# Optimization experiments

Hardware: AMD Instinct MI355X
Metric: run time of the kernel (lower is better)

The kernel has to match this reference:

```python
import jax, jax.numpy as jnp
import numpy as np

B, T, C = 4, 1024, 768
H, HD = 12, 64
E, K, DFF = 16, 2, 3072
EPS = 1e-5


def layernorm(x, w, b):
    mu = jnp.mean(x, axis=-1, keepdims=True)
    xc = x - mu
    var = jnp.mean(xc * xc, axis=-1, keepdims=True)
    return xc * jax.lax.rsqrt(var + EPS) * w + b


def setup_inputs() -> dict:
    key = jax.random.key(0)
    ks = jax.random.split(key, 12)
    s = lambda fan_in: 1.0 / np.sqrt(fan_in)
    return {
        "x": jax.random.normal(ks[0], (B, T, C), jnp.float32),
        "ln1_w": jnp.ones((C,), jnp.float32),
        "ln1_b": jnp.zeros((C,), jnp.float32),
        "W_attn": jax.random.normal(ks[1], (C, 3 * C), jnp.float32) * s(C),
        "b_attn": jnp.zeros((3 * C,), jnp.float32),
        "W_proj": jax.random.normal(ks[2], (C, C), jnp.float32) * s(C),
        "b_proj": jnp.zeros((C,), jnp.float32),
        "ln2_w": jnp.ones((C,), jnp.float32),
        "ln2_b": jnp.zeros((C,), jnp.float32),
        "W_router": jax.random.normal(ks[3], (C, E), jnp.float32) * s(C),
        "W1": jax.random.normal(ks[4], (E, C, DFF), jnp.float32) * s(C),
        "b1": jnp.zeros((E, DFF), jnp.float32),
        "W2": jax.random.normal(ks[5], (E, DFF, C), jnp.float32) * s(DFF),
        "b2": jnp.zeros((E, C), jnp.float32),
    }


def reference(x, ln1_w, ln1_b, W_attn, b_attn, W_proj, b_proj,
              ln2_w, ln2_b, W_router, W1, b1, W2, b2):
    # --- attention sublayer ---
    xn = layernorm(x, ln1_w, ln1_b)
    qkv = xn @ W_attn + b_attn                                  # [B,T,3C]
    q, k, v = jnp.split(qkv, 3, axis=-1)
    q = q.reshape(B, T, H, HD).transpose(0, 2, 1, 3)            # [B,H,T,HD]
    k = k.reshape(B, T, H, HD).transpose(0, 2, 1, 3)
    v = v.reshape(B, T, H, HD).transpose(0, 2, 1, 3)
    att = jnp.einsum('bhqd,bhkd->bhqk', q, k) / np.sqrt(HD)
    causal = jnp.tril(jnp.ones((T, T), bool))
    att = jnp.where(causal, att, -jnp.inf)
    att = jax.nn.softmax(att, axis=-1)
    y = jnp.einsum('bhqk,bhkd->bhqd', att, v)
    y = y.transpose(0, 2, 1, 3).reshape(B, T, C)
    x = x + y @ W_proj + b_proj

    # --- MoE sublayer: dense all-experts with top-k gating mask ---
    xn2 = layernorm(x, ln2_w, ln2_b)
    probs = jax.nn.softmax(xn2 @ W_router, axis=-1)             # [B,T,E]
    top_p, top_idx = jax.lax.top_k(probs, K)                    # [B,T,K]
    gating = jnp.sum(jax.nn.one_hot(top_idx, E, dtype=probs.dtype)
                     * top_p[..., None], axis=-2)               # [B,T,E]
    g = jnp.moveaxis(gating, -1, 0)                             # [E,B,T]

    def body(acc, params):
        W1e, b1e, W2e, b2e, ge = params
        h = jax.nn.gelu(xn2 @ W1e + b1e, approximate=False)     # [B,T,DFF]
        out = h @ W2e + b2e                                     # [B,T,C]
        return acc + ge[..., None] * out, None

    y_moe, _ = jax.lax.scan(body, jnp.zeros_like(x), (W1, b1, W2, b2, g))
    # note: MoELayer returns x + y, and Block adds residual again
    return x + (xn2_residual := 0) + xn2 * 0 + (x * 0) + x * 0 + y_moe + x * 0 if False else x + (x * 0) + y_moe + x * 0 * 0 if False else x + x * 0 + y_moe + (x - x) if False else x + (x + y_moe) - x + (x + y_moe) - (x + y_moe) if False else x + x + y_moe - x if False else (x + (x + y_moe)) - x + (x - x) if False else x + y_moe + x - x if False else _block_out(x, xn2, y_moe)


def _block_out(x, xn2, y_moe):
    # MoELayer.forward returns x_in + y where x_in is ln2 *input* (x here);
    # Block then does x = x + ffn(ln2(x)) -> x + (x + y_moe)? No: MoE input is
    # xn2 = ln2(x), so ffn(ln2(x)) = xn2 + y_moe, and Block adds residual x.
    return x + xn2 + y_moe
```

## Files before the change

### kernel.cpp

```cpp
#include <hip/hip_runtime.h>
#include <math.h>

#define CC    768
#define C3    2304
#define KD    2304
#define LDA2  1536
#define TT    1024
#define BB    4
#define HH    12
#define HD    64
#define EE    16
#define DFFN  3072
#define NTOK  4096
#define NSLOT 8192
#define LDP   136

typedef unsigned short u16;
typedef unsigned int   u32;
typedef __attribute__((ext_vector_type(8))) short short8;
typedef __attribute__((ext_vector_type(4))) float floatx4;

__device__ __forceinline__ u16 f2bf(float f){
  u32 x = __builtin_bit_cast(u32, f);
  x += 0x7fffu + ((x >> 16) & 1u);
  return (u16)(x >> 16);
}
__device__ __forceinline__ u16 f2h(float f){
  _Float16 h = (_Float16)f;
  return __builtin_bit_cast(u16, h);
}
__device__ __forceinline__ float h2f(u16 u){
  return (float)__builtin_bit_cast(_Float16, u);
}
__device__ __forceinline__ float gelu_exact(float v){
  return 0.5f * v * (1.f + erff(v * 0.70710678118654752440f));
}
__device__ __forceinline__ void split2h(float v, u16& h0, u16& h1){
  float vs = v * 64.f;
  h0 = f2h(vs);
  h1 = f2h(vs - h2f(h0));
}
__device__ __forceinline__ void gload_lds16(const void* g, void* l){
  __builtin_amdgcn_global_load_lds(
      (const __attribute__((address_space(1))) void*)g,
      (__attribute__((address_space(3))) void*)l, 16, 0, 0);
}

#define PIPE_WAIT_STEADY  asm volatile("s_waitcnt vmcnt(4) lgkmcnt(0)" ::: "memory")
#define PIPE_WAIT_LAST    asm volatile("s_waitcnt vmcnt(0) lgkmcnt(0)" ::: "memory")
#define PIPE_BARRIER      asm volatile("s_barrier" ::: "memory")

template<int MODE>
__global__ __launch_bounds__(256) void transpose_split(const float* __restrict__ src,
    u16* __restrict__ d0, int R, int Cn)
{
  __shared__ float tile[32][33];
  int z = blockIdx.z;
  const float* s = src + (size_t)z * R * Cn;
  int c0 = blockIdx.x * 32, r0 = blockIdx.y * 32;
  int tx = threadIdx.x & 31, ty = threadIdx.x >> 5;
  #pragma unroll
  for (int j = 0; j < 4; ++j)
    tile[ty + j*8][tx] = s[(size_t)(r0 + ty + j*8) * Cn + c0 + tx];
  __syncthreads();
  #pragma unroll
  for (int j = 0; j < 4; ++j){
    float v = tile[tx][ty + j*8];
    if (MODE == 1){
      u16 h0, h1; split2h(v, h0, h1);
      size_t base = (size_t)(c0 + ty + j*8) * LDA2 + (r0 + tx);
      d0[base] = h0; d0[base + 768] = h1;
    } else {
      d0[(size_t)z * R * Cn + (size_t)(c0 + ty + j*8) * R + r0 + tx] = f2bf(v);
    }
  }
}

template<int MODE>
__global__ __launch_bounds__(256) void ln_kernel(const float* __restrict__ x,
    const float* __restrict__ gw, const float* __restrict__ gb,
    float* __restrict__ of, u16* __restrict__ o0)
{
  int tok = blockIdx.x, tid = threadIdx.x;
  const float* xr = x + (size_t)tok * CC;
  float v0 = xr[tid], v1 = xr[tid + 256], v2 = xr[tid + 512];
  __shared__ float r1[4], r2[4];
  __shared__ float mus, rss;
  float s = v0 + v1 + v2;
  #pragma unroll
  for (int off = 32; off >= 1; off >>= 1) s += __shfl_down(s, off);
  if ((tid & 63) == 0) r1[tid >> 6] = s;
  __syncthreads();
  if (tid == 0) mus = (r1[0] + r1[1] + r1[2] + r1[3]) * (1.f / 768.f);
  __syncthreads();
  float mu = mus;
  float d0 = v0 - mu, d1 = v1 - mu, d2 = v2 - mu;
  float t = d0*d0 + d1*d1 + d2*d2;
  #pragma unroll
  for (int off = 32; off >= 1; off >>= 1) t += __shfl_down(t, off);
  if ((tid & 63) == 0) r2[tid >> 6] = t;
  __syncthreads();
  if (tid == 0) rss = rsqrtf((r2[0] + r2[1] + r2[2] + r2[3]) * (1.f / 768.f) + 1e-5f);
  __syncthreads();
  float rstd = rss;
  float dv[3] = {d0, d1, d2};
  #pragma unroll
  for (int i = 0; i < 3; ++i){
    int c = tid + i * 256;
    float vv = dv[i] * rstd * gw[c] + gb[c];
    if (MODE == 1){
      u16 h0, h1; split2h(vv, h0, h1);
      o0[(size_t)tok * LDA2 + c] = h0;
      o0[(size_t)tok * LDA2 + 768 + c] = h1;
    } else {
      size_t idx = (size_t)tok * CC + c;
      of[idx] = vv;
      o0[idx] = f2bf(vv);
    }
  }
}

__global__ __launch_bounds__(256) void gemm_dense(
    const u16* __restrict__ A, const u16* __restrict__ Bt,
    float* __restrict__ C, const float* __restrict__ bias,
    const float* __restrict__ resid, int N)
{
  __shared__ u16 As[3][128 * 32];
  __shared__ u16 Bs[3][128 * 32];
  int tid = threadIdx.x;
  int lane = tid & 63, wave = tid >> 6;
  int wm = wave & 1, wn = wave >> 1;
  int m0 = blockIdx.y * 128, n0 = blockIdx.x * 128;
  int ra = tid >> 2, ka = (tid & 3) * 8;
  const u16* pa0 = A  + (size_t)(m0 + ra)      * LDA2 + ka;
  const u16* pa1 = A  + (size_t)(m0 + ra + 64) * LDA2 + ka;
  const u16* pb0 = Bt + (size_t)(n0 + ra)      * LDA2 + ka;
  const u16* pb1 = Bt + (size_t)(n0 + ra + 64) * LDA2 + ka;
  floatx4 acc[4][4] = {};
  int el = lane & 15, eq = lane >> 4;

  auto stage = [&](int buf, int k0){
    int ca = (k0 >= 768) ? k0 - 768 : k0;
    int cb = (k0 < 1536) ? k0 : k0 - 1536;
    gload_lds16(pa0 + ca, &As[buf][wave*512]);
    gload_lds16(pa1 + ca, &As[buf][2048 + wave*512]);
    gload_lds16(pb0 + cb, &Bs[buf][wave*512]);
    gload_lds16(pb1 + cb, &Bs[buf][2048 + wave*512]);
  };
  const int nsteps = KD / 32;
  stage(0, 0);
  stage(1, 32);
  int cur = 0;
  for (int i = 0; i < nsteps; ++i){
    __builtin_amdgcn_sched_barrier(0);
    if (i + 1 < nsteps) PIPE_WAIT_STEADY; else PIPE_WAIT_LAST;
    PIPE_BARRIER;
    if (i + 2 < nsteps){
      int nx = cur + 2; if (nx >= 3) nx -= 3;
      stage(nx, (i + 2) * 32);
    }
    short8 fa[4], fb[4];
    #pragma unroll
    for (int t = 0; t < 4; ++t)
      fa[t] = *(const short8*)&As[cur][(size_t)(wm*64 + t*16 + el) * 32 + eq*8];
    #pragma unroll
    for (int t = 0; t < 4; ++t)
      fb[t] = *(const short8*)&Bs[cur][(size_t)(wn*64 + t*16 + el) * 32 + eq*8];
    #pragma unroll
    for (int mt = 0; mt < 4; ++mt)
      #pragma unroll
      for (int nt = 0; nt < 4; ++nt)
        acc[mt][nt] = __builtin_amdgcn_mfma_f32_16x16x32_f16(fa[mt], fb[nt], acc[mt][nt], 0, 0, 0);
    cur = (cur == 2) ? 0 : cur + 1;
  }
  const float ds = 1.f / 4096.f;
  #pragma unroll
  for (int mt = 0; mt < 4; ++mt){
    #pragma unroll
    for (int nt = 0; nt < 4; ++nt){
      int col = n0 + wn*64 + nt*16 + el;
      float bv = bias ? bias[col] : 0.f;
      #pragma unroll
      for (int r = 0; r < 4; ++r){
        int row = m0 + wm*64 + mt*16 + eq*4 + r;
        size_t idx = (size_t)row * N + col;
        float val = acc[mt][nt][r] * ds + bv;
        if (resid) val += resid[idx];
        C[idx] = val;
      }
    }
  }
}

__global__ __launch_bounds__(256) void flash_mfma(const float* __restrict__ qkv,
    u16* __restrict__ yH)
{
  __shared__ u16 Qs[64 * LDP];
  __shared__ u16 Ks[64 * LDP];
  __shared__ u16 Vt[64 * LDP];
  __shared__ u16 Ps[64 * LDP];
  int tid = threadIdx.x;
  int lane = tid & 63, wv = tid >> 6;
  int qi = 15 - blockIdx.x;
  int bh = blockIdx.y;
  int b = bh / HH, h = bh % HH;
  int el = lane & 15, eq = lane >> 4;
  int m0 = wv * 16;
  int row0 = qi * 64;

  {
    int r = tid >> 2, d0 = (tid & 3) * 16;
    const float* src = qkv + (size_t)(b*TT + row0 + r) * C3 + h*HD + d0;
    u16* q0 = &Qs[r * LDP + d0];
    #pragma unroll
    for (int i = 0; i < 16; i += 2){
      u16 a0, a1, b0, b1;
      split2h(src[i], a0, a1);
      split2h(src[i+1], b0, b1);
      *(u32*)&q0[i]      = (u32)a0 | ((u32)b0 << 16);
      *(u32*)&q0[64 + i] = (u32)a1 | ((u32)b1 << 16);
    }
  }
  floatx4 O[4] = {};
  float mrow[4], lrow[4];
  #pragma unroll
  for (int r = 0; r < 4; ++r){ mrow[r] = -1e30f; lrow[r] = 0.f; }

  const float cmul = 0.125f * 1.44269504088896340736f / 4096.f;
  const int ABase[6] = {0,32,0,32,64,96};
  const int BBase[6] = {0,32,64,96,0,32};

  for (int kt = 0; kt <= qi; ++kt){
    __syncthreads();
    {
      int j = tid >> 2, d0 = (tid & 3) * 16;
      const float* src = qkv + (size_t)(b*TT + kt*64 + j) * C3 + CC + h*HD + d0;
      u16* kp = &Ks[j * LDP + d0];
      #pragma unroll
      for (int i = 0; i < 16; i += 2){
        u16 a0, a1, b0, b1;
        split2h(src[i], a0, a1);
        split2h(src[i+1], b0, b1);
        *(u32*)&kp[i]      = (u32)a0 | ((u32)b0 << 16);
        *(u32*)&kp[64 + i] = (u32)a1 | ((u32)b1 << 16);
      }
      int d = tid & 63, kp0 = (tid >> 6) * 16;
      const float* vsrc = qkv + (size_t)(b*TT + kt*64 + kp0) * C3 + 2*CC + h*HD + d;
      u16* vt = &Vt[d * LDP];
      #pragma unroll
      for (int i = 0; i < 16; i += 2){
        u16 a0, a1, b0, b1;
        split2h(vsrc[(size_t)i * C3], a0, a1);
        split2h(vsrc[(size_t)(i+1) * C3], b0, b1);
        *(u32*)&vt[kp0 + i]      = (u32)a0 | ((u32)b0 << 16);
        *(u32*)&vt[64 + kp0 + i] = (u32)a1 | ((u32)b1 << 16);
      }
    }
    __syncthreads();
    floatx4 S[4] = {};
    #pragma unroll
    for (int ks = 0; ks < 6; ++ks){
      short8 fa = *(const short8*)&Qs[(m0 + el) * LDP + ABase[ks] + eq*8];
      short8 fb[4];
      #pragma unroll
      for (int nt = 0; nt < 4; ++nt)
        fb[nt] = *(const short8*)&Ks[(nt*16 + el) * LDP + BBase[ks] + eq*8];
      #pragma unroll
      for (int nt = 0; nt < 4; ++nt)
        S[nt] = __builtin_amdgcn_mfma_f32_16x16x32_f16(fa, fb[nt], S[nt], 0, 0, 0);
    }
    #pragma unroll
    for (int nt = 0; nt < 4; ++nt){
      int kcol = kt*64 + nt*16 + el;
      #pragma unroll
      for (int r = 0; r < 4; ++r){
        int grow = row0 + m0 + eq*4 + r;
        float sv = S[nt][r] * cmul;
        S[nt][r] = (kcol <= grow) ? sv : -1e30f;
      }
    }
    #pragma unroll
    for (int r = 0; r < 4; ++r){
      float tmax = fmaxf(fmaxf(S[0][r], S[1][r]), fmaxf(S[2][r], S[3][r]));
      #pragma unroll
      for (int off = 1; off < 16; off <<= 1) tmax = fmaxf(tmax, __shfl_xor(tmax, off));
      float mnew = fmaxf(mrow[r], tmax);
      float al = exp2f(mrow[r] - mnew);
      mrow[r] = mnew;
      lrow[r] *= al;
      #pragma unroll
      for (int nt = 0; nt < 4; ++nt) O[nt][r] *= al;
      #pragma unroll
      for (int nt = 0; nt < 4; ++nt){
        float p = exp2f(S[nt][r] - mnew);
        lrow[r] += p;
        S[nt][r] = p;
      }
    }
    #pragma unroll
    for (int nt = 0; nt < 4; ++nt){
      #pragma unroll
      for (int r = 0; r < 4; ++r){
        u16 p0, p1; split2h(S[nt][r], p0, p1);
        int rowl = m0 + eq*4 + r;
        Ps[rowl * LDP + nt*16 + el] = p0;
        Ps[rowl * LDP + 64 + nt*16 + el] = p1;
      }
    }
    #pragma unroll
    for (int ks = 0; ks < 6; ++ks){
      short8 fa = *(const short8*)&Ps[(m0 + el) * LDP + ABase[ks] + eq*8];
      short8 fb[4];
      #pragma unroll
      for (int nt = 0; nt < 4; ++nt)
        fb[nt] = *(const short8*)&Vt[(nt*16 + el) * LDP + BBase[ks] + eq*8];
      #pragma unroll
      for (int nt = 0; nt < 4; ++nt)
        O[nt] = __builtin_amdgcn_mfma_f32_16x16x32_f16(fa, fb[nt], O[nt], 0, 0, 0);
    }
  }
  #pragma unroll
  for (int r = 0; r < 4; ++r){
    float l = lrow[r];
    #pragma unroll
    for (int off = 1; off < 16; off <<= 1) l += __shfl_xor(l, off);
    float inv = 1.f / (l * 4096.f);
    int grow = row0 + m0 + eq*4 + r;
    u16* dst = yH + (size_t)(b*TT + grow) * LDA2 + h*HD;
    #pragma unroll
    for (int nt = 0; nt < 4; ++nt){
      float yv = O[nt][r] * inv;
      u16 y0, y1; split2h(yv, y0, y1);
      dst[nt*16 + el] = y0;
      dst[768 + nt*16 + el] = y1;
    }
  }
}

__global__ __launch_bounds__(256) void router_kernel(const float* __restrict__ xn2,
    const float* __restrict__ Wr, int* __restrict__ eids, float* __restrict__ wts)
{
  int wave = threadIdx.x >> 6, lane = threadIdx.x & 63;
  int tok = blockIdx.x * 4 + wave;
  int g = lane >> 4, e = lane & 15;
  const float* xr = xn2 + (size_t)tok * CC;
  float s = 0.f;
  for (int c4 = 0; c4 < 192; ++c4){
    int c = c4 * 4 + g;
    s += xr[c] * Wr[c * EE + e];
  }
  s += __shfl_xor(s, 16);
  s += __shfl_xor(s, 32);
  float mx = s;
  #pragma unroll
  for (int off = 1; off < 16; off <<= 1) mx = fmaxf(mx, __shfl_xor(mx, off));
  float p = expf(s - mx);
  float Z = p;
  #pragma unroll
  for (int off = 1; off < 16; off <<= 1) Z += __shfl_xor(Z, off);
  p /= Z;
  float best = -1.f; int bi = 0;
  for (int ee = 0; ee < 16; ++ee){
    float pe = __shfl(p, ee);
    if (pe > best){ best = pe; bi = ee; }
  }
  float sec = -1.f; int si = 0;
  for (int ee = 0; ee < 16; ++ee){
    float pe = __shfl(p, ee);
    if (ee != bi && pe > sec){ sec = pe; si = ee; }
  }
  if (lane == 0){
    eids[tok*2] = bi;  eids[tok*2+1] = si;
    wts [tok*2] = best; wts[tok*2+1] = sec;
  }
}

__global__ __launch_bounds__(256) void moe_count(const int* __restrict__ eids,
    int* __restrict__ counts, int* __restrict__ offs, int* __restrict__ curs)
{
  __shared__ int lc[EE];
  int tid = threadIdx.x;
  if (tid < EE) lc[tid] = 0;
  __syncthreads();
  for (int i = tid; i < NSLOT; i += 256) atomicAdd(&lc[eids[i]], 1);
  __syncthreads();
  if (tid == 0){
    int run = 0;
    for (int e = 0; e < EE; ++e){
      counts[e] = lc[e]; offs[e] = run; curs[e] = run; run += lc[e];
    }
    offs[EE] = run;
  }
}

__global__ __launch_bounds__(256) void moe_scatter(const int* __restrict__ eids,
    const float* __restrict__ wts, int* __restrict__ curs,
    int* __restrict__ rowmap, float* __restrict__ wgtm)
{
  int i = blockIdx.x * 256 + threadIdx.x;
  int e = eids[i];
  int pos = atomicAdd(&curs[e], 1);
  rowmap[pos] = i >> 1;
  wgtm[pos] = wts[i];
}

__global__ __launch_bounds__(256) void add2(const float* __restrict__ a,
    const float* __restrict__ b, float* __restrict__ o, int n)
{
  int i = blockIdx.x * 256 + threadIdx.x;
  if (i < n) o[i] = a[i] + b[i];
}

__global__ __launch_bounds__(256) void gemm_moe1(
    const u16* __restrict__ Xb, const u16* __restrict__ W1t, const float* __restrict__ b1,
    u16* __restrict__ H, const int* __restrict__ counts, const int* __restrict__ offs,
    const int* __restrict__ rowmap)
{
  int e = blockIdx.z;
  int cnt = counts[e];
  int m0 = blockIdx.y * 128;
  if (m0 >= cnt) return;
  int off = offs[e];
  int n0 = blockIdx.x * 128;
  const u16* Bt = W1t + (size_t)e * DFFN * CC;
  __shared__ u16 As[3][128 * 32];
  __shared__ u16 Bs[3][128 * 32];
  int tid = threadIdx.x;
  int lane = tid & 63, wave = tid >> 6;
  int wm = wave & 1, wn = wave >> 1;
  int ra = tid >> 2, ka = (tid & 3) * 8;
  int r0 = m0 + ra, r1i = m0 + ra + 64;
  int rr0 = (r0  < cnt) ? r0  : cnt - 1;
  int rr1 = (r1i < cnt) ? r1i : cnt - 1;
  const u16* pa0 = Xb + (size_t)rowmap[off + rr0] * CC + ka;
  const u16* pa1 = Xb + (size_t)rowmap[off + rr1] * CC + ka;
  const u16* pb0 = Bt + (size_t)(n0 + ra)      * CC + ka;
  const u16* pb1 = Bt + (size_t)(n0 + ra + 64) * CC + ka;
  floatx4 acc[4][4] = {};
  int el = lane & 15, eq = lane >> 4;

  auto stage = [&](int buf, int k0){
    gload_lds16(pa0 + k0, &As[buf][wave*512]);
    gload_lds16(pa1 + k0, &As[buf][2048 + wave*512]);
    gload_lds16(pb0 + k0, &Bs[buf][wave*512]);
    gload_lds16(pb1 + k0, &Bs[buf][2048 + wave*512]);
  };
  const int nsteps = CC / 32;
  stage(0, 0);
  stage(1, 32);
  int cur = 0;
  for (int i = 0; i < nsteps; ++i){
    __builtin_amdgcn_sched_barrier(0);
    if (i + 1 < nsteps) PIPE_WAIT_STEADY; else PIPE_WAIT_LAST;
    PIPE_BARRIER;
    if (i + 2 < nsteps){
      int nx = cur + 2; if (nx >= 3) nx -= 3;
      stage(nx, (i + 2) * 32);
    }
    short8 fa[4], fb[4];
    #pragma unroll
    for (int t = 0; t < 4; ++t)
      fa[t] = *(const short8*)&As[cur][(size_t)(wm*64 + t*16 + el) * 32 + eq*8];
    #pragma unroll
    for (int t = 0; t < 4; ++t)
      fb[t] = *(const short8*)&Bs[cur][(size_t)(wn*64 + t*16 + el) * 32 + eq*8];
    #pragma unroll
    for (int mt = 0; mt < 4; ++mt)
      #pragma unroll
      for (int nt = 0; nt < 4; ++nt)
        acc[mt][nt] = __builtin_amdgcn_mfma_f32_16x16x32_bf16(fa[mt], fb[nt], acc[mt][nt], 0, 0, 0);
    cur = (cur == 2) ? 0 : cur + 1;
  }
  #pragma unroll
  for (int mt = 0; mt < 4; ++mt){
    #pragma unroll
    for (int nt = 0; nt < 4; ++nt){
      int col = n0 + wn*64 + nt*16 + el;
      float bv = b1[(size_t)e * DFFN + col];
      #pragma unroll
      for (int r = 0; r < 4; ++r){
        int row = m0 + wm*64 + mt*16 + eq*4 + r;
        if (row < cnt)
          H[(size_t)(off + row) * DFFN + col] = f2bf(gelu_exact(acc[mt][nt][r] + bv));
      }
    }
  }
}

#define KSPL 2
__global__ __launch_bounds__(256) void gemm_moe2(
    const u16* __restrict__ H, const u16* __restrict__ W2t, const float* __restrict__ b2,
    float* __restrict__ Out, const int* __restrict__ counts, const int* __restrict__ offs,
    const int* __restrict__ rowmap, const float* __restrict__ wgtm)
{
  int e = blockIdx.z;
  int cnt = counts[e];
  int m0 = blockIdx.y * 128;
  if (m0 >= cnt) return;
  int off = offs[e];
  int bx = blockIdx.x;
  int n0 = (bx % 6) * 128;
  int ksp = bx / 6;
  const u16* Bt = W2t + (size_t)e * CC * DFFN;
  __shared__ u16 As[3][128 * 32];
  __shared__ u16 Bs[3][128 * 32];
  int tid = threadIdx.x;
  int lane = tid & 63, wave = tid >> 6;
  int wm = wave & 1, wn = wave >> 1;
  int ra = tid >> 2, ka = (tid & 3) * 8;
  int r0 = m0 + ra, r1i = m0 + ra + 64;
  int rr0 = (r0  < cnt) ? r0  : cnt - 1;
  int rr1 = (r1i < cnt) ? r1i : cnt - 1;
  const u16* pa0 = H + (size_t)(off + rr0) * DFFN + ka;
  const u16* pa1 = H + (size_t)(off + rr1) * DFFN + ka;
  const u16* pb0 = Bt + (size_t)(n0 + ra)      * DFFN + ka;
  const u16* pb1 = Bt + (size_t)(n0 + ra + 64) * DFFN + ka;
  floatx4 acc[4][4] = {};
  int el = lane & 15, eq = lane >> 4;
  int kbeg = ksp * (DFFN / KSPL);

  auto stage = [&](int buf, int k0){
    gload_lds16(pa0 + k0, &As[buf][wave*512]);
    gload_lds16(pa1 + k0, &As[buf][2048 + wave*512]);
    gload_lds16(pb0 + k0, &Bs[buf][wave*512]);
    gload_lds16(pb1 + k0, &Bs[buf][2048 + wave*512]);
  };
  const int nsteps = (DFFN / KSPL) / 32;
  stage(0, kbeg);
  stage(1, kbeg + 32);
  int cur = 0;
  for (int i = 0; i < nsteps; ++i){
    __builtin_amdgcn_sched_barrier(0);
    if (i + 1 < nsteps) PIPE_WAIT_STEADY; else PIPE_WAIT_LAST;
    PIPE_BARRIER;
    if (i + 2 < nsteps){
      int nx = cur + 2; if (nx >= 3) nx -= 3;
      stage(nx, kbeg + (i + 2) * 32);
    }
    short8 fa[4], fb[4];
    #pragma unroll
    for (int t = 0; t < 4; ++t)
      fa[t] = *(const short8*)&As[cur][(size_t)(wm*64 + t*16 + el) * 32 + eq*8];
    #pragma unroll
    for (int t = 0; t < 4; ++t)
      fb[t] = *(const short8*)&Bs[cur][(size_t)(wn*64 + t*16 + el) * 32 + eq*8];
    #pragma unroll
    for (int mt = 0; mt < 4; ++mt)
      #pragma unroll
      for (int nt = 0; nt < 4; ++nt)
        acc[mt][nt] = __builtin_amdgcn_mfma_f32_16x16x32_bf16(fa[mt], fb[nt], acc[mt][nt], 0, 0, 0);
    cur = (cur == 2) ? 0 : cur + 1;
  }
  #pragma unroll
  for (int mt = 0; mt < 4; ++mt){
    #pragma unroll
    for (int nt = 0; nt < 4; ++nt){
      int col = n0 + wn*64 + nt*16 + el;
      float bv = (ksp == 0) ? b2[(size_t)e * CC + col] : 0.f;
      #pragma unroll
      for (int r = 0; r < 4; ++r){
        int row = m0 + wm*64 + mt*16 + eq*4 + r;
        if (row < cnt){
          int slot = off + row;
          int tok = rowmap[slot];
          float wv = wgtm[slot];
          atomicAdd(&Out[(size_t)tok * CC + col], wv * (acc[mt][nt][r] + bv));
        }
      }
    }
  }
}

extern "C" void kernel_launch(void* const* d_in, const int* in_sizes, int n_in,
                              void* d_out, int out_size, void* d_ws, size_t ws_size,
                              hipStream_t stream)
{
  const float* x     = (const float*)d_in[0];
  const float* ln1w  = (const float*)d_in[1];
  const float* ln1b  = (const float*)d_in[2];
  const float* Wattn = (const float*)d_in[3];
  const float* battn = (const float*)d_in[4];
  const float* Wproj = (const float*)d_in[5];
  const float* bproj = (const float*)d_in[6];
  const float* ln2w  = (const float*)d_in[7];
  const float* ln2b  = (const float*)d_in[8];
  const float* Wrout = (const float*)d_in[9];
  const float* W1    = (const float*)d_in[10];
  const float* b1    = (const float*)d_in[11];
  const float* W2    = (const float*)d_in[12];
  const float* b2    = (const float*)d_in[13];
  float* out = (float*)d_out;

  char* w = (char*)d_ws;
  auto alloc = [&](size_t bytes)->char* {
    char* p = w; w += (bytes + 255) & ~(size_t)255; return p;
  };
  u16* watp  = (u16*)alloc((size_t)C3 * LDA2 * 2);
  u16* wptp  = (u16*)alloc((size_t)CC * LDA2 * 2);
  u16* w1t   = (u16*)alloc((size_t)EE * DFFN * CC * 2);
  u16* w2t   = (u16*)alloc((size_t)EE * CC * DFFN * 2);
  u16* xH    = (u16*)alloc((size_t)NTOK * LDA2 * 2);
  float* qkv = (float*)alloc((size_t)NTOK * C3 * 4);
  u16* yH    = (u16*)alloc((size_t)NTOK * LDA2 * 2);
  u16* Hbuf  = (u16*)alloc((size_t)NSLOT * DFFN * 2);
  float* x2    = (float*)alloc((size_t)NTOK * CC * 4);
  float* xn2   = (float*)alloc((size_t)NTOK * CC * 4);
  u16*   xn2b  = (u16*)alloc((size_t)NTOK * CC * 2);
  int*   eids  = (int*)alloc(NSLOT * 4);
  float* wts   = (float*)alloc(NSLOT * 4);
  int* counts  = (int*)alloc(256);
  int* offs    = (int*)alloc(256);
  int* curs    = (int*)alloc(256);
  int* rowmap  = (int*)alloc(NSLOT * 4);
  float* wgtm  = (float*)alloc(NSLOT * 4);

  hipLaunchKernelGGL((transpose_split<1>), dim3(C3/32, CC/32, 1), dim3(256), 0, stream,
                     Wattn, watp, CC, C3);
  hipLaunchKernelGGL((transpose_split<1>), dim3(CC/32, CC/32, 1), dim3(256), 0, stream,
                     Wproj, wptp, CC, CC);
  hipLaunchKernelGGL((transpose_split<0>), dim3(DFFN/32, CC/32, EE), dim3(256), 0, stream,
                     W1, w1t, CC, DFFN);
  hipLaunchKernelGGL((transpose_split<0>), dim3(CC/32, DFFN/32, EE), dim3(256), 0, stream,
                     W2, w2t, DFFN, CC);
  hipLaunchKernelGGL((ln_kernel<1>), dim3(NTOK), dim3(256), 0, stream,
                     x, ln1w, ln1b, (float*)nullptr, xH);
  hipLaunchKernelGGL(gemm_dense, dim3(C3/128, NTOK/128), dim3(256), 0, stream,
                     xH, watp, qkv, battn, (const float*)nullptr, C3);
  hipLaunchKernelGGL(flash_mfma, dim3(16, BB*HH), dim3(256), 0, stream, qkv, yH);
  hipLaunchKernelGGL(gemm_dense, dim3(CC/128, NTOK/128), dim3(256), 0, stream,
                     yH, wptp, x2, bproj, x, CC);
  hipLaunchKernelGGL((ln_kernel<0>), dim3(NTOK), dim3(256), 0, stream,
                     x2, ln2w, ln2b, xn2, xn2b);
  hipLaunchKernelGGL(router_kernel, dim3(NTOK/4), dim3(256), 0, stream, xn2, Wrout, eids, wts);
  hipLaunchKernelGGL(moe_count, dim3(1), dim3(256), 0, stream, eids, counts, offs, curs);
  hipLaunchKernelGGL(moe_scatter, dim3(NSLOT/256), dim3(256), 0, stream, eids, wts, curs, rowmap, wgtm);
  hipLaunchKernelGGL(add2, dim3(NTOK*CC/256), dim3(256), 0, stream, x2, xn2, out, NTOK*CC);
  hipLaunchKernelGGL(gemm_moe1, dim3(DFFN/128, 32, EE), dim3(256), 0, stream,
                     xn2b, w1t, b1, Hbuf, counts, offs, rowmap);
  hipLaunchKernelGGL(gemm_moe2, dim3(6*KSPL, 32, EE), dim3(256), 0, stream,
                     Hbuf, w2t, b2, out, counts, offs, rowmap, wgtm);
}
```

Measured before the change: 954.1 us.

## Replace MoE atomic scatter-add with slot buffer and per-token finalize kernel

The second expert GEMM now writes each split-K partial result, bias included, as plain stores into a per-slot buffer. It no longer does weighted atomicAdds into the output rows of each token. The scatter kernel records each token's slot positions, and a new finalize kernel gathers the two slots and two K-splits per token, applies the gate weights, and adds the residual terms. That replaces the separate add2 kernel. This removes contended fp32 atomics, at the cost of writing and reading an extra buffer of about 50MB. That buffer is carved from xH, which only works if xH and qkv are laid out contiguously in the workspace.

```diff
diff --git a/kernel.cpp b/kernel.cpp
--- a/kernel.cpp
+++ b/kernel.cpp
@@ -395,20 +395,13 @@
 
 __global__ __launch_bounds__(256) void moe_scatter(const int* __restrict__ eids,
     const float* __restrict__ wts, int* __restrict__ curs,
-    int* __restrict__ rowmap, float* __restrict__ wgtm)
+    int* __restrict__ rowmap, int* __restrict__ invmap)
 {
   int i = blockIdx.x * 256 + threadIdx.x;
   int e = eids[i];
   int pos = atomicAdd(&curs[e], 1);
   rowmap[pos] = i >> 1;
-  wgtm[pos] = wts[i];
-}
-
-__global__ __launch_bounds__(256) void add2(const float* __restrict__ a,
-    const float* __restrict__ b, float* __restrict__ o, int n)
-{
-  int i = blockIdx.x * 256 + threadIdx.x;
-  if (i < n) o[i] = a[i] + b[i];
+  invmap[i] = pos;
 }
 
 __global__ __launch_bounds__(256) void gemm_moe1(
@@ -490,8 +483,7 @@
 #define KSPL 2
 __global__ __launch_bounds__(256) void gemm_moe2(
     const u16* __restrict__ H, const u16* __restrict__ W2t, const float* __restrict__ b2,
-    float* __restrict__ Out, const int* __restrict__ counts, const int* __restrict__ offs,
-    const int* __restrict__ rowmap, const float* __restrict__ wgtm)
+    float* __restrict__ Y, const int* __restrict__ counts, const int* __restrict__ offs)
 {
   int e = blockIdx.z;
   int cnt = counts[e];
@@ -560,14 +552,31 @@
       #pragma unroll
       for (int r = 0; r < 4; ++r){
         int row = m0 + wm*64 + mt*16 + eq*4 + r;
-        if (row < cnt){
-          int slot = off + row;
-          int tok = rowmap[slot];
-          float wv = wgtm[slot];
-          atomicAdd(&Out[(size_t)tok * CC + col], wv * (acc[mt][nt][r] + bv));
-        }
-      }
-    }
+        if (row < cnt)
+          Y[((size_t)ksp * NSLOT + off + row) * CC + col] = acc[mt][nt][r] + bv;
+      }
+    }
+  }
+}
+
+__global__ __launch_bounds__(256) void moe_finalize(const float* __restrict__ x2,
+    const float* __restrict__ xn2, const float* __restrict__ Y,
+    const int* __restrict__ invmap, const float* __restrict__ wts,
+    float* __restrict__ out)
+{
+  int t = blockIdx.x, tid = threadIdx.x;
+  int s0 = invmap[t*2], s1 = invmap[t*2 + 1];
+  float w0 = wts[t*2],  w1 = wts[t*2 + 1];
+  const float* y00 = Y + (size_t)s0 * CC;
+  const float* y01 = Y + ((size_t)NSLOT + s0) * CC;
+  const float* y10 = Y + (size_t)s1 * CC;
+  const float* y11 = Y + ((size_t)NSLOT + s1) * CC;
+  size_t base = (size_t)t * CC;
+  #pragma unroll
+  for (int i = 0; i < 3; ++i){
+    int c = tid + i * 256;
+    out[base + c] = x2[base + c] + xn2[base + c]
+                  + w0 * (y00[c] + y01[c]) + w1 * (y10[c] + y11[c]);
   }
 }
 
@@ -612,7 +621,8 @@
   int* offs    = (int*)alloc(256);
   int* curs    = (int*)alloc(256);
   int* rowmap  = (int*)alloc(NSLOT * 4);
-  float* wgtm  = (float*)alloc(NSLOT * 4);
+  int* invmap  = (int*)alloc(NSLOT * 4);
+  float* Ybuf = (float*)xH;
 
   hipLaunchKernelGGL((transpose_split<1>), dim3(C3/32, CC/32, 1), dim3(256), 0, stream,
                      Wattn, watp, CC, C3);
@@ -633,10 +643,11 @@
                      x2, ln2w, ln2b, xn2, xn2b);
   hipLaunchKernelGGL(router_kernel, dim3(NTOK/4), dim3(256), 0, stream, xn2, Wrout, eids, wts);
   hipLaunchKernelGGL(moe_count, dim3(1), dim3(256), 0, stream, eids, counts, offs, curs);
-  hipLaunchKernelGGL(moe_scatter, dim3(NSLOT/256), dim3(256), 0, stream, eids, wts, curs, rowmap, wgtm);
-  hipLaunchKernelGGL(add2, dim3(NTOK*CC/256), dim3(256), 0, stream, x2, xn2, out, NTOK*CC);
+  hipLaunchKernelGGL(moe_scatter, dim3(NSLOT/256), dim3(256), 0, stream, eids, wts, curs, rowmap, invmap);
   hipLaunchKernelGGL(gemm_moe1, dim3(DFFN/128, 32, EE), dim3(256), 0, stream,
                      xn2b, w1t, b1, Hbuf, counts, offs, rowmap);
   hipLaunchKernelGGL(gemm_moe2, dim3(6*KSPL, 32, EE), dim3(256), 0, stream,
-                     Hbuf, w2t, b2, out, counts, offs, rowmap, wgtm);
-}
+                     Hbuf, w2t, b2, Ybuf, counts, offs);
+  hipLaunchKernelGGL(moe_finalize, dim3(NTOK), dim3(256), 0, stream,
+                     x2, xn2, Ybuf, invmap, wts, out);
+}
```

Measured after the change: 909.6 us. -4.7%, faster.
